# Optimization experiments

Measured on AMD Instinct MI355X. Metric: run time of the kernel, lower is better.

## Reference

```python
import math
import jax, jax.numpy as jnp
import numpy as np

N_HEAD = 16
HEAD_DIM = 128


def _rope(x, cos, sin):
    # x: (B,T,H,D); cos,sin: (T,1,D/2) broadcast over B,H
    d = x.shape[-1] // 2
    x1, x2 = x[..., :d], x[..., d:]
    return jnp.concatenate([x1 * cos + x2 * sin, -x1 * sin + x2 * cos], axis=-1)


def _rms_norm(x, eps=1e-6):
    return x * jax.lax.rsqrt(jnp.mean(x * x, axis=-1, keepdims=True) + eps)


def setup_inputs() -> dict:
    key = jax.random.key(0)
    ks = jax.random.split(key, 9)
    B, T, C = 2, 2048, 2048
    scale = 1.0 / math.sqrt(C)
    return {
        "x": jax.random.normal(ks[0], (B, T, C), jnp.float32),
        "ve": jax.random.normal(ks[1], (B, T, C), jnp.float32),
        "Wq": jax.random.normal(ks[2], (C, C), jnp.float32) * scale,
        "Wk": jax.random.normal(ks[3], (C, C), jnp.float32) * scale,
        "Wv": jax.random.normal(ks[4], (C, C), jnp.float32) * scale,
        "Wproj": jax.random.normal(ks[5], (C, C), jnp.float32) * scale,
        "Wgate": jax.random.normal(ks[6], (N_HEAD, 12), jnp.float32) * (1.0 / math.sqrt(12.0)),
        "cos": jax.random.uniform(ks[7], (T, 1, HEAD_DIM // 2), jnp.float32),
        "sin": jax.random.uniform(ks[8], (T, 1, HEAD_DIM // 2), jnp.float32),
        "window_left": 1024,
    }


def reference(x, ve, Wq, Wk, Wv, Wproj, Wgate, cos, sin, window_left):
    B, T, C = x.shape
    H, D = N_HEAD, HEAD_DIM

    # Linear projections (torch Linear: x @ W.T)
    q = (x @ Wq.T).reshape(B, T, H, D)
    k = (x @ Wk.T).reshape(B, T, H, D)
    v = (x @ Wv.T).reshape(B, T, H, D)

    # value-embedding gating (has_ve layer)
    gate = 3.0 * jax.nn.sigmoid(x[..., :12] @ Wgate.T)  # (B,T,H)
    v = v + gate[..., None] * ve.reshape(B, T, H, D)

    # rope + qk rms-norm * 1.2
    q = _rms_norm(_rope(q, cos, sin)) * 1.2
    k = _rms_norm(_rope(k, cos, sin)) * 1.2

    # windowed causal mask
    row = jnp.arange(T)[:, None]
    col = jnp.arange(T)[None, :]
    mask = row >= col
    if 0 < window_left < T:
        mask = mask & (row - col <= window_left)
    bias = jnp.where(mask, 0.0, -1e9).astype(x.dtype)  # (T,T)

    scale = 1.0 / math.sqrt(D)
    att = jnp.einsum("bqhd,bkhd->bhqk", q, k) * scale + bias[None, None]
    att = jax.nn.softmax(att, axis=-1)
    y = jnp.einsum("bhqk,bkhd->bqhd", att, v).reshape(B, T, H * D)
    return y @ Wproj.T
```

## Files before the change

kernel.cpp:

```cpp
#include <hip/hip_runtime.h>
#include <hip/hip_bf16.h>
#include <cstdint>

#define N_HEAD 16
#define HEAD_DIM 128

typedef __bf16 bf16;
typedef __bf16 bf16x8 __attribute__((ext_vector_type(8)));
typedef __bf16 bf16x4 __attribute__((ext_vector_type(4)));
typedef float f32x4 __attribute__((ext_vector_type(4)));

__device__ __forceinline__ void gload_lds16(const void* g, void* l) {
  auto gp = reinterpret_cast<const __attribute__((address_space(1))) char*>(
      reinterpret_cast<uintptr_t>(g));
  auto lp = reinterpret_cast<__attribute__((address_space(3))) char*>(
      reinterpret_cast<uintptr_t>(l));
  __builtin_amdgcn_global_load_lds(gp, lp, 16, 0, 0);
}

__global__ __launch_bounds__(256) void cvt_bf16(const float* __restrict__ in,
                                                bf16* __restrict__ out, int n4) {
  int i = blockIdx.x * 256 + threadIdx.x;
  if (i >= n4) return;
  const float4 f = reinterpret_cast<const float4*>(in)[i];
  bf16x4 o;
  o.x = (bf16)f.x; o.y = (bf16)f.y; o.z = (bf16)f.z; o.w = (bf16)f.w;
  reinterpret_cast<bf16x4*>(out)[i] = o;
}

template <typename OutT>
__global__ __launch_bounds__(256) void gemm_bt(
    const bf16* __restrict__ A, const bf16* __restrict__ Bt,
    OutT* __restrict__ C, int M, int N, int K) {
  __shared__ __align__(16) bf16 As[128 * 32];
  __shared__ __align__(16) bf16 Bs[128 * 32];
  const int tid = threadIdx.x;
  const int lane = tid & 63;
  const int wave = tid >> 6;
  const int wm = (wave >> 1) * 64;
  const int wn = (wave & 1) * 64;
  const int lr = lane & 15;
  const int lk = (lane >> 4) * 8;

  const bf16* Ab = A + (size_t)blockIdx.y * 128 * K;
  const bf16* Bb = Bt + (size_t)blockIdx.x * 128 * K;

  const int r0 = tid >> 2;
  const int c0 = (tid & 3) * 8;

  f32x4 acc[4][4] = {};

  for (int k0 = 0; k0 < K; k0 += 32) {
    __syncthreads();
    gload_lds16(Ab + (size_t)r0 * K + k0 + c0, As + (size_t)tid * 8);
    gload_lds16(Ab + (size_t)(r0 + 64) * K + k0 + c0, As + (size_t)(256 + tid) * 8);
    gload_lds16(Bb + (size_t)r0 * K + k0 + c0, Bs + (size_t)tid * 8);
    gload_lds16(Bb + (size_t)(r0 + 64) * K + k0 + c0, Bs + (size_t)(256 + tid) * 8);
    __syncthreads();

    bf16x8 a[4], b[4];
#pragma unroll
    for (int i = 0; i < 4; ++i)
      a[i] = *reinterpret_cast<const bf16x8*>(As + (wm + i * 16 + lr) * 32 + lk);
#pragma unroll
    for (int j = 0; j < 4; ++j)
      b[j] = *reinterpret_cast<const bf16x8*>(Bs + (wn + j * 16 + lr) * 32 + lk);
#pragma unroll
    for (int i = 0; i < 4; ++i)
#pragma unroll
      for (int j = 0; j < 4; ++j)
        acc[i][j] = __builtin_amdgcn_mfma_f32_16x16x32_bf16(a[i], b[j], acc[i][j], 0, 0, 0);
  }

  const int orow = blockIdx.y * 128 + wm + (lane >> 4) * 4;
  const int ocol = blockIdx.x * 128 + wn + lr;
#pragma unroll
  for (int i = 0; i < 4; ++i)
#pragma unroll
    for (int j = 0; j < 4; ++j)
#pragma unroll
      for (int r = 0; r < 4; ++r)
        C[(size_t)(orow + i * 16 + r) * N + (ocol + j * 16)] = (OutT)acc[i][j][r];
}

__global__ __launch_bounds__(256) void rope_rms(
    bf16* __restrict__ qkv, const float* __restrict__ cs,
    const float* __restrict__ sn, int T) {
  const int C = N_HEAD * HEAD_DIM;
  const int S = 3 * C;
  const int bt = blockIdx.x;
  const int t = bt % T;
  const int wave = threadIdx.x >> 6;
  const int lane = threadIdx.x & 63;
  const int h = blockIdx.y * 4 + wave;
  bf16* p = qkv + (size_t)bt * S + (blockIdx.z ? C : 0) + h * HEAD_DIM;
  const float oscale = blockIdx.z ? 1.2f : 0.15302091809294977f;
  const float c = cs[t * 64 + lane];
  const float s = sn[t * 64 + lane];
  const float x1 = (float)p[lane];
  const float x2 = (float)p[lane + 64];
  const float r1 = x1 * c + x2 * s;
  const float r2 = x2 * c - x1 * s;
  float ss = r1 * r1 + r2 * r2;
#pragma unroll
  for (int m = 1; m < 64; m <<= 1) ss += __shfl_xor(ss, m);
  const float sc = oscale * rsqrtf(ss * (1.0f / 128.0f) + 1e-6f);
  p[lane] = (bf16)(r1 * sc);
  p[lane + 64] = (bf16)(r2 * sc);
}

__global__ __launch_bounds__(256) void gate_transpose(
    const bf16* __restrict__ qkv, const float* __restrict__ x,
    const float* __restrict__ ve, const float* __restrict__ Wg,
    bf16* __restrict__ vT, int T) {
  const int C = N_HEAD * HEAD_DIM;
  const int S = 3 * C;
  const int t0 = blockIdx.x * 64;
  const int c0 = blockIdx.y * 64;
  const int b = blockIdx.z;
  const int h = c0 >> 7;

  __shared__ float gs[64];
  __shared__ __align__(16) bf16 tile[64][72];

  if (threadIdx.x < 64) {
    const float* xr = x + (size_t)(b * T + t0 + threadIdx.x) * C;
    float a = 0.f;
#pragma unroll
    for (int j = 0; j < 12; ++j) a += xr[j] * Wg[h * 12 + j];
    gs[threadIdx.x] = 3.f / (1.f + __expf(-a));
  }
  __syncthreads();

  {
    const int r = threadIdx.x >> 2;
    const int cc = (threadIdx.x & 3) * 16;
    const size_t vrow = (size_t)(b * T + t0 + r) * S + 2 * C + c0 + cc;
    const size_t erow = (size_t)(b * T + t0 + r) * C + c0 + cc;
    bf16x8 a0 = *reinterpret_cast<const bf16x8*>(qkv + vrow);
    bf16x8 a1 = *reinterpret_cast<const bf16x8*>(qkv + vrow + 8);
    const float g = gs[r];
    bf16x8 o0, o1;
#pragma unroll
    for (int i = 0; i < 8; ++i) o0[i] = (bf16)((float)a0[i] + g * ve[erow + i]);
#pragma unroll
    for (int i = 0; i < 8; ++i) o1[i] = (bf16)((float)a1[i] + g * ve[erow + 8 + i]);
    *reinterpret_cast<bf16x8*>(&tile[r][cc]) = o0;
    *reinterpret_cast<bf16x8*>(&tile[r][cc + 8]) = o1;
  }
  __syncthreads();
  {
    const int dr = threadIdx.x >> 2;
    const int tc = (threadIdx.x & 3) * 16;
    bf16x8 o0, o1;
#pragma unroll
    for (int i = 0; i < 8; ++i) o0[i] = tile[tc + i][dr];
#pragma unroll
    for (int i = 0; i < 8; ++i) o1[i] = tile[tc + 8 + i][dr];
    const size_t orow =
        ((size_t)((b * N_HEAD + h) * HEAD_DIM) + (c0 & 127) + dr) * T + t0 + tc;
    *reinterpret_cast<bf16x8*>(vT + orow) = o0;
    *reinterpret_cast<bf16x8*>(vT + orow + 8) = o1;
  }
}

__global__ __launch_bounds__(256, 3) void attn(
    const bf16* __restrict__ qkv, const bf16* __restrict__ vT,
    bf16* __restrict__ y, const int* __restrict__ wptr, int T) {
  const int C = N_HEAD * HEAD_DIM;
  const int S = 3 * C;
  const int qb = blockIdx.x * 64;
  const int h = blockIdx.y;
  const int b = blockIdx.z;
  const int tid = threadIdx.x;
  const int wave = tid >> 6;
  const int lane = tid & 63;
  const int lm = lane & 15;
  const int quad = lane >> 4;

  const int w = wptr[0];
  const int W = (w > 0 && w < T) ? w : (1 << 30);

  __shared__ __align__(16) bf16 Ks[4][64][32];
  __shared__ __align__(16) bf16 Vs[2][128][32];
  __shared__ __align__(16) bf16 Pb[4][16][72];

  const bf16* kb = qkv + (size_t)b * T * S + C + (size_t)h * HEAD_DIM;
  const bf16* vb = vT + (size_t)((b * N_HEAD + h) * HEAD_DIM) * T;

  const int qg0 = qb + wave * 16;
  const bf16* qrow = qkv + (size_t)(b * T + qg0 + lm) * S + h * HEAD_DIM;
  bf16x8 qf[4];
#pragma unroll
  for (int c = 0; c < 4; ++c)
    qf[c] = *reinterpret_cast<const bf16x8*>(qrow + c * 32 + quad * 8);

  float mrun = -1e30f, lrun = 0.f;
  f32x4 oacc[8] = {};

  int kstart = qb - W;
  if (kstart < 0) kstart = 0;
  kstart &= ~63;
  const int qr = qg0 + lm;

  const int sr = tid >> 2;
  const int sc = (tid & 3) * 8;

  for (int kc = kstart; kc <= qb + 63; kc += 64) {
    __syncthreads();
#pragma unroll
    for (int c = 0; c < 4; ++c)
      gload_lds16(kb + (size_t)(kc + sr) * S + c * 32 + sc, &Ks[c][0][0] + tid * 8);
#pragma unroll
    for (int c2 = 0; c2 < 2; ++c2)
#pragma unroll
      for (int i = 0; i < 2; ++i)
        gload_lds16(vb + (size_t)(i * 64 + sr) * T + kc + c2 * 32 + sc,
                    &Vs[c2][i * 64][0] + tid * 8);
    __syncthreads();

    f32x4 st[4] = {};
#pragma unroll
    for (int g = 0; g < 4; ++g)
#pragma unroll
      for (int c = 0; c < 4; ++c) {
        const bf16x8 kf =
            *reinterpret_cast<const bf16x8*>(&Ks[c][g * 16 + lm][quad * 8]);
        st[g] = __builtin_amdgcn_mfma_f32_16x16x32_bf16(kf, qf[c], st[g], 0, 0, 0);
      }
    float mx = -1e30f;
#pragma unroll
    for (int g = 0; g < 4; ++g)
#pragma unroll
      for (int r = 0; r < 4; ++r) {
        const int key = kc + g * 16 + quad * 4 + r;
        const bool valid = (key <= qr) && (qr - key <= W);
        st[g][r] = valid ? st[g][r] : -1e30f;
        mx = fmaxf(mx, st[g][r]);
      }
    mx = fmaxf(mx, __shfl_xor(mx, 16));
    mx = fmaxf(mx, __shfl_xor(mx, 32));
    const float mnew = fmaxf(mrun, mx);
    const float alpha = __builtin_amdgcn_exp2f(mrun - mnew);
    mrun = mnew;
    float rs = 0.f;
#pragma unroll
    for (int g = 0; g < 4; ++g) {
      bf16x4 pk;
#pragma unroll
      for (int r = 0; r < 4; ++r) {
        const float p = __builtin_amdgcn_exp2f(st[g][r] - mnew);
        rs += p;
        pk[r] = (bf16)p;
      }
      *reinterpret_cast<bf16x4*>(&Pb[wave][lm][g * 16 + quad * 4]) = pk;
    }
    rs += __shfl_xor(rs, 16);
    rs += __shfl_xor(rs, 32);
    lrun = lrun * alpha + rs;
#pragma unroll
    for (int dc = 0; dc < 8; ++dc)
#pragma unroll
      for (int r = 0; r < 4; ++r) oacc[dc][r] *= alpha;
#pragma unroll
    for (int c2 = 0; c2 < 2; ++c2) {
      const bf16x8 pf =
          *reinterpret_cast<const bf16x8*>(&Pb[wave][lm][c2 * 32 + quad * 8]);
#pragma unroll
      for (int dc = 0; dc < 8; ++dc) {
        const bf16x8 vf =
            *reinterpret_cast<const bf16x8*>(&Vs[c2][dc * 16 + lm][quad * 8]);
        oacc[dc] = __builtin_amdgcn_mfma_f32_16x16x32_bf16(vf, pf, oacc[dc], 0, 0, 0);
      }
    }
  }

  const float inv = 1.f / lrun;
  bf16* yr = y + (size_t)(b * T + qg0 + lm) * C + h * HEAD_DIM;
#pragma unroll
  for (int dc = 0; dc < 8; ++dc) {
    bf16x4 o;
#pragma unroll
    for (int r = 0; r < 4; ++r) o[r] = (bf16)(oacc[dc][r] * inv);
    *reinterpret_cast<bf16x4*>(yr + dc * 16 + quad * 4) = o;
  }
}

extern "C" void kernel_launch(void* const* d_in, const int* in_sizes, int n_in,
                              void* d_out, int out_size, void* d_ws, size_t ws_size,
                              hipStream_t stream) {
  const float* x  = (const float*)d_in[0];
  const float* ve = (const float*)d_in[1];
  const float* Wq = (const float*)d_in[2];
  const float* Wk = (const float*)d_in[3];
  const float* Wv = (const float*)d_in[4];
  const float* Wp = (const float*)d_in[5];
  const float* Wg = (const float*)d_in[6];
  const float* cs = (const float*)d_in[7];
  const float* sn = (const float*)d_in[8];
  const int*   wl = (const int*)d_in[9];
  float* out = (float*)d_out;

  const int C = N_HEAD * HEAD_DIM;
  const int T = in_sizes[7] / (HEAD_DIM / 2);
  const int B = in_sizes[0] / (T * C);
  const int M = B * T;

  bf16* xb   = (bf16*)d_ws;
  bf16* wqkv = xb   + (size_t)M * C;
  bf16* wpb  = wqkv + (size_t)3 * C * C;
  bf16* qkv  = wpb  + (size_t)C * C;
  bf16* ybuf = qkv  + (size_t)3 * M * C;
  bf16* vTb  = xb;

  const int nx4 = M * C / 4, nw4 = C * C / 4;
  cvt_bf16<<<(nx4 + 255) / 256, 256, 0, stream>>>(x, xb, nx4);
  cvt_bf16<<<(nw4 + 255) / 256, 256, 0, stream>>>(Wq, wqkv, nw4);
  cvt_bf16<<<(nw4 + 255) / 256, 256, 0, stream>>>(Wk, wqkv + (size_t)C * C, nw4);
  cvt_bf16<<<(nw4 + 255) / 256, 256, 0, stream>>>(Wv, wqkv + (size_t)2 * C * C, nw4);
  cvt_bf16<<<(nw4 + 255) / 256, 256, 0, stream>>>(Wp, wpb, nw4);

  gemm_bt<bf16><<<dim3(3 * C / 128, M / 128), 256, 0, stream>>>(xb, wqkv, qkv, M, 3 * C, C);

  rope_rms<<<dim3(M, N_HEAD / 4, 2), 256, 0, stream>>>(qkv, cs, sn, T);
  gate_transpose<<<dim3(T / 64, C / 64, B), 256, 0, stream>>>(qkv, x, ve, Wg, vTb, T);
  attn<<<dim3(T / 64, N_HEAD, B), 256, 0, stream>>>(qkv, vTb, ybuf, wl, T);

  gemm_bt<float><<<dim3(C / 128, M / 128), 256, 0, stream>>>(ybuf, wpb, out, M, C, C);
}
```

Measured before the change: 472.1 us.

## Process two query tiles per attention block and merge bf16 conversion launches

```diff
diff --git a/kernel.cpp b/kernel.cpp
--- a/kernel.cpp
+++ b/kernel.cpp
@@ -18,9 +18,21 @@
   __builtin_amdgcn_global_load_lds(gp, lp, 16, 0, 0);
 }
 
-__global__ __launch_bounds__(256) void cvt_bf16(const float* __restrict__ in,
-                                                bf16* __restrict__ out, int n4) {
-  int i = blockIdx.x * 256 + threadIdx.x;
+__global__ __launch_bounds__(256) void cvt_all(
+    const float* __restrict__ x, const float* __restrict__ Wq,
+    const float* __restrict__ Wk, const float* __restrict__ Wv,
+    const float* __restrict__ Wp, bf16* __restrict__ xb,
+    bf16* __restrict__ wqkv, bf16* __restrict__ wpb, int nx4, int nw4) {
+  const int z = blockIdx.z;
+  const float* in;
+  bf16* out;
+  int n4;
+  if (z == 0)      { in = x;  out = xb;  n4 = nx4; }
+  else if (z == 1) { in = Wq; out = wqkv;                     n4 = nw4; }
+  else if (z == 2) { in = Wk; out = wqkv + (size_t)nw4 * 4;   n4 = nw4; }
+  else if (z == 3) { in = Wv; out = wqkv + (size_t)nw4 * 8;   n4 = nw4; }
+  else             { in = Wp; out = wpb;  n4 = nw4; }
+  const int i = blockIdx.x * 256 + threadIdx.x;
   if (i >= n4) return;
   const float4 f = reinterpret_cast<const float4*>(in)[i];
   bf16x4 o;
@@ -164,12 +176,12 @@
   }
 }
 
-__global__ __launch_bounds__(256, 3) void attn(
+__global__ __launch_bounds__(256, 2) void attn(
     const bf16* __restrict__ qkv, const bf16* __restrict__ vT,
     bf16* __restrict__ y, const int* __restrict__ wptr, int T) {
   const int C = N_HEAD * HEAD_DIM;
   const int S = 3 * C;
-  const int qb = blockIdx.x * 64;
+  const int qb = blockIdx.x * 128;
   const int h = blockIdx.y;
   const int b = blockIdx.z;
   const int tid = threadIdx.x;
@@ -188,25 +200,27 @@
   const bf16* kb = qkv + (size_t)b * T * S + C + (size_t)h * HEAD_DIM;
   const bf16* vb = vT + (size_t)((b * N_HEAD + h) * HEAD_DIM) * T;
 
-  const int qg0 = qb + wave * 16;
-  const bf16* qrow = qkv + (size_t)(b * T + qg0 + lm) * S + h * HEAD_DIM;
-  bf16x8 qf[4];
-#pragma unroll
-  for (int c = 0; c < 4; ++c)
-    qf[c] = *reinterpret_cast<const bf16x8*>(qrow + c * 32 + quad * 8);
-
-  float mrun = -1e30f, lrun = 0.f;
-  f32x4 oacc[8] = {};
+  const int qt[2] = {qb + wave * 16, qb + 64 + wave * 16};
+  bf16x8 qf[2][4];
+#pragma unroll
+  for (int t = 0; t < 2; ++t) {
+    const bf16* qrow = qkv + (size_t)(b * T + qt[t] + lm) * S + h * HEAD_DIM;
+#pragma unroll
+    for (int c = 0; c < 4; ++c)
+      qf[t][c] = *reinterpret_cast<const bf16x8*>(qrow + c * 32 + quad * 8);
+  }
+
+  float mrun[2] = {-1e30f, -1e30f}, lrun[2] = {0.f, 0.f};
+  f32x4 oacc[2][8] = {};
 
   int kstart = qb - W;
   if (kstart < 0) kstart = 0;
   kstart &= ~63;
-  const int qr = qg0 + lm;
 
   const int sr = tid >> 2;
   const int sc = (tid & 3) * 8;
 
-  for (int kc = kstart; kc <= qb + 63; kc += 64) {
+  for (int kc = kstart; kc <= qb + 127; kc += 64) {
     __syncthreads();
 #pragma unroll
     for (int c = 0; c < 4; ++c)
@@ -219,70 +233,80 @@
                     &Vs[c2][i * 64][0] + tid * 8);
     __syncthreads();
 
-    f32x4 st[4] = {};
-#pragma unroll
-    for (int g = 0; g < 4; ++g)
-#pragma unroll
-      for (int c = 0; c < 4; ++c) {
-        const bf16x8 kf =
-            *reinterpret_cast<const bf16x8*>(&Ks[c][g * 16 + lm][quad * 8]);
-        st[g] = __builtin_amdgcn_mfma_f32_16x16x32_bf16(kf, qf[c], st[g], 0, 0, 0);
+#pragma unroll
+    for (int t = 0; t < 2; ++t) {
+      const int q0 = qt[t];
+      if (kc > q0 + 15 || kc + 63 < q0 - W) continue;
+      const int qr = q0 + lm;
+
+      f32x4 st[4] = {};
+#pragma unroll
+      for (int g = 0; g < 4; ++g)
+#pragma unroll
+        for (int c = 0; c < 4; ++c) {
+          const bf16x8 kf =
+              *reinterpret_cast<const bf16x8*>(&Ks[c][g * 16 + lm][quad * 8]);
+          st[g] = __builtin_amdgcn_mfma_f32_16x16x32_bf16(kf, qf[t][c], st[g], 0, 0, 0);
+        }
+      float mx = -1e30f;
+#pragma unroll
+      for (int g = 0; g < 4; ++g)
+#pragma unroll
+        for (int r = 0; r < 4; ++r) {
+          const int key = kc + g * 16 + quad * 4 + r;
+          const bool valid = (key <= qr) && (qr - key <= W);
+          st[g][r] = valid ? st[g][r] : -1e30f;
+          mx = fmaxf(mx, st[g][r]);
+        }
+      mx = fmaxf(mx, __shfl_xor(mx, 16));
+      mx = fmaxf(mx, __shfl_xor(mx, 32));
+      const float mnew = fmaxf(mrun[t], mx);
+      const float alpha = __builtin_amdgcn_exp2f(mrun[t] - mnew);
+      mrun[t] = mnew;
+      float rs = 0.f;
+#pragma unroll
+      for (int g = 0; g < 4; ++g) {
+        bf16x4 pk;
+#pragma unroll
+        for (int r = 0; r < 4; ++r) {
+          const float p = __builtin_amdgcn_exp2f(st[g][r] - mnew);
+          rs += p;
+          pk[r] = (bf16)p;
+        }
+        *reinterpret_cast<bf16x4*>(&Pb[wave][lm][g * 16 + quad * 4]) = pk;
       }
-    float mx = -1e30f;
-#pragma unroll
-    for (int g = 0; g < 4; ++g)
-#pragma unroll
-      for (int r = 0; r < 4; ++r) {
-        const int key = kc + g * 16 + quad * 4 + r;
-        const bool valid = (key <= qr) && (qr - key <= W);
-        st[g][r] = valid ? st[g][r] : -1e30f;
-        mx = fmaxf(mx, st[g][r]);
-      }
-    mx = fmaxf(mx, __shfl_xor(mx, 16));
-    mx = fmaxf(mx, __shfl_xor(mx, 32));
-    const float mnew = fmaxf(mrun, mx);
-    const float alpha = __builtin_amdgcn_exp2f(mrun - mnew);
-    mrun = mnew;
-    float rs = 0.f;
-#pragma unroll
-    for (int g = 0; g < 4; ++g) {
-      bf16x4 pk;
-#pragma unroll
-      for (int r = 0; r < 4; ++r) {
-        const float p = __builtin_amdgcn_exp2f(st[g][r] - mnew);
-        rs += p;
-        pk[r] = (bf16)p;
-      }
-      *reinterpret_cast<bf16x4*>(&Pb[wave][lm][g * 16 + quad * 4]) = pk;
-    }
-    rs += __shfl_xor(rs, 16);
-    rs += __shfl_xor(rs, 32);
-    lrun = lrun * alpha + rs;
-#pragma unroll
-    for (int dc = 0; dc < 8; ++dc)
-#pragma unroll
-      for (int r = 0; r < 4; ++r) oacc[dc][r] *= alpha;
-#pragma unroll
-    for (int c2 = 0; c2 < 2; ++c2) {
-      const bf16x8 pf =
-          *reinterpret_cast<const bf16x8*>(&Pb[wave][lm][c2 * 32 + quad * 8]);
-#pragma unroll
-      for (int dc = 0; dc < 8; ++dc) {
-        const bf16x8 vf =
-            *reinterpret_cast<const bf16x8*>(&Vs[c2][dc * 16 + lm][quad * 8]);
-        oacc[dc] = __builtin_amdgcn_mfma_f32_16x16x32_bf16(vf, pf, oacc[dc], 0, 0, 0);
+      rs += __shfl_xor(rs, 16);
+      rs += __shfl_xor(rs, 32);
+      lrun[t] = lrun[t] * alpha + rs;
+#pragma unroll
+      for (int dc = 0; dc < 8; ++dc)
+#pragma unroll
+        for (int r = 0; r < 4; ++r) oacc[t][dc][r] *= alpha;
+#pragma unroll
+      for (int c2 = 0; c2 < 2; ++c2) {
+        const bf16x8 pf =
+            *reinterpret_cast<const bf16x8*>(&Pb[wave][lm][c2 * 32 + quad * 8]);
+#pragma unroll
+        for (int dc = 0; dc < 8; ++dc) {
+          const bf16x8 vf =
+              *reinterpret_cast<const bf16x8*>(&Vs[c2][dc * 16 + lm][quad * 8]);
+          oacc[t][dc] = __builtin_amdgcn_mfma_f32_16x16x32_bf16(vf, pf, oacc[t][dc], 0, 0, 0);
+        }
       }
     }
   }
 
-  const float inv = 1.f / lrun;
-  bf16* yr = y + (size_t)(b * T + qg0 + lm) * C + h * HEAD_DIM;
-#pragma unroll
-  for (int dc = 0; dc < 8; ++dc) {
-    bf16x4 o;
-#pragma unroll
-    for (int r = 0; r < 4; ++r) o[r] = (bf16)(oacc[dc][r] * inv);
-    *reinterpret_cast<bf16x4*>(yr + dc * 16 + quad * 4) = o;
+#pragma unroll
+  for (int t = 0; t < 2; ++t) {
+    const float inv = 1.f / lrun[t];
+    bf16* yr = y + (size_t)(b * T + qt[t] + lm) * C + h * HEAD_DIM;
+#pragma unroll
+    for (int dc = 0; dc < 8; ++dc) {
+      bf16x4 o;
+#pragma unroll
+      for (int r = 0; r < 4; ++r) o[r] = (bf16)(oacc[t][dc][r] * inv);
+      *reinterpret_cast<bf16x4*>(yr + dc * 16 + quad * 4) = o;
+    }
   }
 }
 
@@ -314,17 +338,14 @@
   bf16* vTb  = xb;
 
   const int nx4 = M * C / 4, nw4 = C * C / 4;
-  cvt_bf16<<<(nx4 + 255) / 256, 256, 0, stream>>>(x, xb, nx4);
-  cvt_bf16<<<(nw4 + 255) / 256, 256, 0, stream>>>(Wq, wqkv, nw4);
-  cvt_bf16<<<(nw4 + 255) / 256, 256, 0, stream>>>(Wk, wqkv + (size_t)C * C, nw4);
-  cvt_bf16<<<(nw4 + 255) / 256, 256, 0, stream>>>(Wv, wqkv + (size_t)2 * C * C, nw4);
-  cvt_bf16<<<(nw4 + 255) / 256, 256, 0, stream>>>(Wp, wpb, nw4);
+  cvt_all<<<dim3((nx4 + 255) / 256, 1, 5), 256, 0, stream>>>(
+      x, Wq, Wk, Wv, Wp, xb, wqkv, wpb, nx4, nw4);
 
   gemm_bt<bf16><<<dim3(3 * C / 128, M / 128), 256, 0, stream>>>(xb, wqkv, qkv, M, 3 * C, C);
 
   rope_rms<<<dim3(M, N_HEAD / 4, 2), 256, 0, stream>>>(qkv, cs, sn, T);
   gate_transpose<<<dim3(T / 64, C / 64, B), 256, 0, stream>>>(qkv, x, ve, Wg, vTb, T);
-  attn<<<dim3(T / 64, N_HEAD, B), 256, 0, stream>>>(qkv, vTb, ybuf, wl, T);
+  attn<<<dim3(T / 128, N_HEAD, B), 256, 0, stream>>>(qkv, vTb, ybuf, wl, T);
 
   gemm_bt<float><<<dim3(C / 128, M / 128), 256, 0, stream>>>(ybuf, wpb, out, M, C, C);
 }
```

After: 448.4 us. 1.05x faster.
